# Optimization experiments

Hardware: AMD Instinct MI355X
Metric: run time of the kernel (lower is better)

The kernel has to match this reference:

```python
import jax, jax.numpy as jnp
import numpy as np

B, C_IN, T = 64, 9, 4096
HIDDEN, OUT = 128, 10
NEW_T = T // 4            # two MaxPool1d(2) stages
N_NODES = B * NEW_T       # 65536 flattened nodes
N_EDGES = 524288


def setup_inputs() -> dict:
    key = jax.random.key(0)
    ks = jax.random.split(key, 8)
    def w(k, sh, fan):
        return jax.random.normal(k, sh, jnp.float32) * (1.0 / np.sqrt(fan))
    return {
        "x": jax.random.normal(ks[0], (B, C_IN, T), jnp.float32),
        "edge_index": jax.random.randint(ks[1], (2, N_EDGES), 0, N_NODES, dtype=jnp.int32),
        "conv1_w": w(ks[2], (16, C_IN, 5), C_IN * 5),
        "conv1_b": jnp.zeros((16,), jnp.float32),
        "conv2_w": w(ks[3], (32, 16, 5), 16 * 5),
        "conv2_b": jnp.zeros((32,), jnp.float32),
        "gcn1_w": w(ks[4], (32, HIDDEN), 32),
        "gcn1_b": jnp.zeros((HIDDEN,), jnp.float32),
        "gcn2_w": w(ks[5], (HIDDEN, HIDDEN), HIDDEN),
        "gcn2_b": jnp.zeros((HIDDEN,), jnp.float32),
        "cls_w": w(ks[6], (HIDDEN, OUT), HIDDEN),
        "cls_b": jnp.zeros((OUT,), jnp.float32),
    }


def _conv1d(x, w, b):
    # x: [B, C, T], w: [O, I, K], 'same' padding (pad=2, k=5)
    y = jax.lax.conv_general_dilated(x, w, (1,), [(2, 2)],
                                     dimension_numbers=("NCH", "OIH", "NCH"))
    return y + b[None, :, None]


def _maxpool2(x):
    return jax.lax.reduce_window(x, -jnp.inf, jax.lax.max, (1, 1, 2), (1, 1, 2), "VALID")


def _gcn(x, w, b, src, dst):
    # PyG GCNConv: add self-loops, symmetric D^{-1/2}(A+I)D^{-1/2} X W + b
    h = x @ w
    deg = jnp.zeros((N_NODES,), x.dtype).at[dst].add(1.0) + 1.0  # +1 for self-loop
    dinv = jax.lax.rsqrt(deg)
    coef = dinv[src] * dinv[dst]                      # [E]
    agg = jnp.zeros_like(h).at[dst].add(h[src] * coef[:, None])
    agg = agg + h * (dinv * dinv)[:, None]            # self-loop contribution
    return agg + b


def reference(x, edge_index, conv1_w, conv1_b, conv2_w, conv2_b,
              gcn1_w, gcn1_b, gcn2_w, gcn2_b, cls_w, cls_b):
    h = _maxpool2(jax.nn.relu(_conv1d(x, conv1_w, conv1_b)))   # [B,16,T/2]
    h = _maxpool2(jax.nn.relu(_conv1d(h, conv2_w, conv2_b)))   # [B,32,T/4]
    feats = h.transpose(0, 2, 1).reshape(-1, 32)               # [B*NEW_T, 32]
    src, dst = edge_index[0], edge_index[1]
    g = jax.nn.relu(_gcn(feats, gcn1_w, gcn1_b, src, dst))
    g = jax.nn.relu(_gcn(g, gcn2_w, gcn2_b, src, dst))
    pooled = g.reshape(B, NEW_T, HIDDEN).mean(axis=1)          # mean over nodes per graph
    return pooled @ cls_w + cls_b                              # [B, OUT]
```

## Files before the change

kernel.cpp:

```cpp
#include <hip/hip_runtime.h>
#include <hip/hip_bf16.h>

typedef __hip_bfloat16 bf16;
typedef unsigned short ushort8_v __attribute__((ext_vector_type(8)));
typedef short bf16x8 __attribute__((ext_vector_type(8)));
typedef float f32x4 __attribute__((ext_vector_type(4)));
typedef float f32x2 __attribute__((ext_vector_type(2)));

#define N_B     64
#define C_IN    9
#define T0      4096
#define C1      16
#define T1      2048
#define C2      32
#define T2      1024
#define N_NODES 65536
#define N_EDGES 524288
#define HID     128
#define OUT_C   10
#define SLOT_CAP 32

__device__ __forceinline__ float us2f(unsigned short u) {
  union { unsigned int i; float f; } c; c.i = ((unsigned int)u) << 16; return c.f;
}
__device__ __forceinline__ unsigned short f2us(float f) {
  bf16 h = __float2bfloat16(f);
  unsigned short u;
  __builtin_memcpy(&u, &h, 2);
  return u;
}
__device__ __forceinline__ unsigned char f2fp8(float f) {
  int p = __builtin_amdgcn_cvt_pk_fp8_f32(f, f, 0, false);
  return (unsigned char)(p & 0xFF);
}
__device__ __forceinline__ void fp8w_to_f32x4(unsigned int w, float* out) {
  f32x2 lo = __builtin_amdgcn_cvt_pk_f32_fp8((int)w, false);
  f32x2 hi = __builtin_amdgcn_cvt_pk_f32_fp8((int)w, true);
  out[0] = lo[0]; out[1] = lo[1]; out[2] = hi[0]; out[3] = hi[1];
}

__global__ __launch_bounds__(256) void conv1_scatter_kernel(const float* __restrict__ x, const float* __restrict__ w1,
                                                            const float* __restrict__ b1,
                                                            const int* __restrict__ ei, int* __restrict__ cnt,
                                                            unsigned short* __restrict__ slots,
                                                            unsigned short* __restrict__ y1,
                                                            const float* __restrict__ W1, const float* __restrict__ W2,
                                                            unsigned short* __restrict__ W1T,
                                                            unsigned short* __restrict__ W2T,
                                                            float* __restrict__ pooled)
{
  __shared__ float sx[C_IN * 136];
  __shared__ float sw[45 * 17];
  __shared__ float sb[C1];
  int tid = threadIdx.x;
  if (blockIdx.x < 2048) {
    int e = blockIdx.x * 256 + tid;
    int d = ei[N_EDGES + e];
    int s = ei[e];
    int r = atomicAdd(&cnt[d], 1);
    if (r < SLOT_CAP) slots[((size_t)d << 5) + r] = (unsigned short)s;
    return;
  }
  if (blockIdx.x >= 4096) {
    int blk = blockIdx.x - 4096;
    if (blk < 16) {
      int base = blk * 1024 + tid * 4;
      #pragma unroll
      for (int i = 0; i < 4; ++i) {
        int idx = base + i;
        int j = idx >> 7, k = idx & 127;
        W2T[j * HID + k] = f2us(W2[(size_t)k * HID + j]);
      }
    } else {
      #pragma unroll
      for (int i = 0; i < 16; ++i) {
        int idx = tid * 16 + i;
        int j = idx >> 5, k = idx & 31;
        W1T[j * 32 + k] = f2us(W1[(size_t)k * HID + j]);
      }
      float4 z4 = make_float4(0.f, 0.f, 0.f, 0.f);
      for (int i = tid; i < N_B * HID / 4; i += 256)
        ((float4*)pooled)[i] = z4;
    }
    return;
  }
  int blk = blockIdx.x - 2048;
  int b = blk >> 5;
  int P0 = (blk & 31) << 6;
  int t0 = 2 * P0 - 2;
  for (int i = tid; i < C_IN * 132; i += 256) {
    int c = i / 132, j = i % 132;
    int t = t0 + j;
    sx[c * 136 + j] = (t >= 0 && t < T0) ? x[(size_t)(b * C_IN + c) * T0 + t] : 0.f;
  }
  for (int i = tid; i < C1 * 45; i += 256) sw[(i % 45) * 17 + i / 45] = w1[i];
  if (tid < C1) sb[tid] = b1[tid];
  __syncthreads();

  int o = tid & 15, pg = tid >> 4;
  float bias = sb[o];
  float a[8];
  #pragma unroll
  for (int i = 0; i < 8; ++i) a[i] = bias;
  #pragma unroll
  for (int c = 0; c < C_IN; ++c) {
    float xv[12];
    #pragma unroll
    for (int q = 0; q < 3; ++q)
      *(float4*)&xv[4 * q] = *(const float4*)&sx[c * 136 + 8 * pg + 4 * q];
    const float* wr = &sw[(c * 5) * 17 + o];
    float w0 = wr[0], w1_ = wr[17], w2_ = wr[34], w3_ = wr[51], w4_ = wr[68];
    #pragma unroll
    for (int m = 0; m < 8; ++m)
      a[m] += xv[m]*w0 + xv[m+1]*w1_ + xv[m+2]*w2_ + xv[m+3]*w3_ + xv[m+4]*w4_;
  }
  ushort4 r;
  r.x = f2us(fmaxf(fmaxf(a[0], a[1]), 0.f));
  r.y = f2us(fmaxf(fmaxf(a[2], a[3]), 0.f));
  r.z = f2us(fmaxf(fmaxf(a[4], a[5]), 0.f));
  r.w = f2us(fmaxf(fmaxf(a[6], a[7]), 0.f));
  *(ushort4*)&y1[(size_t)(b * C1 + o) * T1 + P0 + 4 * pg] = r;
}

__global__ __launch_bounds__(256) void conv2_kernel(const unsigned short* __restrict__ y1, const float* __restrict__ w2,
                                                    const float* __restrict__ b2, const int* __restrict__ cnt,
                                                    unsigned short* __restrict__ feats)
{
  __shared__ float sy[C1 * 72];
  __shared__ float sw[80 * 33];
  __shared__ float sb[C2];
  int tid = threadIdx.x;
  int b = blockIdx.x >> 5;
  int Q0 = (blockIdx.x & 31) << 5;
  int t0 = 2 * Q0 - 2;
  for (int i = tid; i < C1 * 68; i += 256) {
    int c = i / 68, j = i % 68;
    int t = t0 + j;
    sy[c * 72 + j] = (t >= 0 && t < T1) ? us2f(y1[(size_t)(b * C1 + c) * T1 + t]) : 0.f;
  }
  for (int i = tid; i < C2 * 80; i += 256) sw[(i % 80) * 33 + i / 80] = w2[i];
  if (tid < C2) sb[tid] = b2[tid];
  __syncthreads();

  int o = tid & 31, pg = tid >> 5;
  float bias = sb[o];
  float a[8];
  #pragma unroll
  for (int i = 0; i < 8; ++i) a[i] = bias;
  #pragma unroll
  for (int c = 0; c < C1; ++c) {
    float yv[12];
    #pragma unroll
    for (int q = 0; q < 3; ++q)
      *(float4*)&yv[4 * q] = *(const float4*)&sy[c * 72 + 8 * pg + 4 * q];
    const float* wr = &sw[(c * 5) * 33 + o];
    float w0 = wr[0], w1_ = wr[33], w2_ = wr[66], w3_ = wr[99], w4_ = wr[132];
    #pragma unroll
    for (int m = 0; m < 8; ++m)
      a[m] += yv[m]*w0 + yv[m+1]*w1_ + yv[m+2]*w2_ + yv[m+3]*w3_ + yv[m+4]*w4_;
  }
  #pragma unroll
  for (int i = 0; i < 4; ++i) {
    int node = (b << 10) + Q0 + 4 * pg + i;
    float dv = rsqrtf((float)cnt[node] + 1.0f);
    feats[(size_t)node * C2 + o] = f2us(fmaxf(fmaxf(a[2*i], a[2*i+1]), 0.f) * dv);
  }
}

__global__ __launch_bounds__(256) void gemm12_kernel(const unsigned short* __restrict__ F,
                                                     const int* __restrict__ cnt,
                                                     const unsigned short* __restrict__ slots,
                                                     const unsigned short* __restrict__ W1T,
                                                     const float* __restrict__ gb1,
                                                     const unsigned short* __restrict__ W2T,
                                                     unsigned char* __restrict__ Hb)
{
  __shared__ unsigned short sG[64 * 132];
  int tid = threadIdx.x;
  int w = tid >> 6, l = tid & 63;
  int lr = l & 15, lk = l >> 4;
  int n0b = blockIdx.x << 6;
  int jb = w << 5;

  {
    int nb = w << 4;
    int node = n0b + nb + lr;
    int cn = cnt[node];
    float dn = rsqrtf((float)cn + 1.0f);
    int koff = lk << 3;
    float accf[8];
    {
      ushort8_v r = *(const ushort8_v*)(F + (size_t)node * C2 + koff);
      #pragma unroll
      for (int k = 0; k < 8; ++k) accf[k] = us2f(r[k]);
    }
    const unsigned short* sl = slots + ((size_t)node << 5);
    int e1 = min(cn, SLOT_CAP);
    int e = 0;
    for (; e + 4 <= e1; e += 4) {
      int s0 = sl[e], s1 = sl[e + 1], s2 = sl[e + 2], s3 = sl[e + 3];
      ushort8_v r0 = *(const ushort8_v*)(F + (size_t)s0 * C2 + koff);
      ushort8_v r1 = *(const ushort8_v*)(F + (size_t)s1 * C2 + koff);
      ushort8_v r2 = *(const ushort8_v*)(F + (size_t)s2 * C2 + koff);
      ushort8_v r3 = *(const ushort8_v*)(F + (size_t)s3 * C2 + koff);
      #pragma unroll
      for (int k = 0; k < 8; ++k)
        accf[k] += (us2f(r0[k]) + us2f(r1[k])) + (us2f(r2[k]) + us2f(r3[k]));
    }
    for (; e < e1; ++e) {
      int s0 = sl[e];
      ushort8_v r0 = *(const ushort8_v*)(F + (size_t)s0 * C2 + koff);
      #pragma unroll
      for (int k = 0; k < 8; ++k) accf[k] += us2f(r0[k]);
    }
    bf16x8 af;
    #pragma unroll
    for (int k = 0; k < 8; ++k) af[k] = (short)f2us(accf[k] * dn);

    #pragma unroll
    for (int jt = 0; jt < 8; ++jt) {
      bf16x8 bfr = *(const bf16x8*)((const short*)W1T + (jt * 16 + lr) * 32 + lk * 8);
      f32x4 acc = {0.f, 0.f, 0.f, 0.f};
      acc = __builtin_amdgcn_mfma_f32_16x16x32_bf16(af, bfr, acc, 0, 0, 0);
      float bj = gb1[jt * 16 + lr];
      #pragma unroll
      for (int r = 0; r < 4; ++r)
        sG[(nb + lk * 4 + r) * 132 + jt * 16 + lr] = f2us(fmaxf(acc[r] + bj, 0.f));
    }
  }

  bf16x8 bfr[2][4];
  #pragma unroll
  for (int jtt = 0; jtt < 2; ++jtt)
    #pragma unroll
    for (int ks = 0; ks < 4; ++ks)
      bfr[jtt][ks] = *(const bf16x8*)((const short*)W2T + (size_t)(jb + jtt * 16 + lr) * HID + ks * 32 + lk * 8);

  __syncthreads();

  {
    #pragma unroll
    for (int nt = 0; nt < 4; ++nt) {
      bf16x8 afr[4];
      #pragma unroll
      for (int ks = 0; ks < 4; ++ks)
        afr[ks] = *(const bf16x8*)((const short*)sG + (nt * 16 + lr) * 132 + ks * 32 + lk * 8);
      int rowb = n0b + nt * 16 + lk * 4;
      int4 c4 = *(const int4*)&cnt[rowb];
      float dvr[4] = { rsqrtf((float)c4.x + 1.f), rsqrtf((float)c4.y + 1.f),
                       rsqrtf((float)c4.z + 1.f), rsqrtf((float)c4.w + 1.f) };
      #pragma unroll
      for (int jtt = 0; jtt < 2; ++jtt) {
        f32x4 acc = {0.f, 0.f, 0.f, 0.f};
        #pragma unroll
        for (int ks = 0; ks < 4; ++ks)
          acc = __builtin_amdgcn_mfma_f32_16x16x32_bf16(afr[ks], bfr[jtt][ks], acc, 0, 0, 0);
        #pragma unroll
        for (int r = 0; r < 4; ++r)
          Hb[(size_t)(rowb + r) * HID + jb + jtt * 16 + lr] = f2fp8(acc[r] * dvr[r]);
      }
    }
  }
}

__global__ __launch_bounds__(256) void agg2_pool_kernel(const unsigned char* __restrict__ Hb, const int* __restrict__ cnt,
                                                        const unsigned short* __restrict__ slots,
                                                        const float* __restrict__ bias, float* __restrict__ pooled)
{
  __shared__ float red[16][HID];
  int tid = threadIdx.x;
  int g = tid >> 4;
  int jq = (tid & 15) << 3;
  int node = (blockIdx.x << 4) + g;
  int cn = cnt[node];
  float dn = rsqrtf((float)cn + 1.0f);
  float acc[8];
  {
    uint2 v = *(const uint2*)(Hb + (size_t)node * HID + jq);
    fp8w_to_f32x4(v.x, &acc[0]);
    fp8w_to_f32x4(v.y, &acc[4]);
  }
  const unsigned short* sl = slots + ((size_t)node << 5);
  int e1 = min(cn, SLOT_CAP);
  int e = 0;
  for (; e + 4 <= e1; e += 4) {
    uint2 v0 = *(const uint2*)(Hb + (size_t)sl[e]     * HID + jq);
    uint2 v1 = *(const uint2*)(Hb + (size_t)sl[e + 1] * HID + jq);
    uint2 v2 = *(const uint2*)(Hb + (size_t)sl[e + 2] * HID + jq);
    uint2 v3 = *(const uint2*)(Hb + (size_t)sl[e + 3] * HID + jq);
    float t0[8], t1[8], t2[8], t3[8];
    fp8w_to_f32x4(v0.x, &t0[0]); fp8w_to_f32x4(v0.y, &t0[4]);
    fp8w_to_f32x4(v1.x, &t1[0]); fp8w_to_f32x4(v1.y, &t1[4]);
    fp8w_to_f32x4(v2.x, &t2[0]); fp8w_to_f32x4(v2.y, &t2[4]);
    fp8w_to_f32x4(v3.x, &t3[0]); fp8w_to_f32x4(v3.y, &t3[4]);
    #pragma unroll
    for (int k = 0; k < 8; ++k)
      acc[k] += (t0[k] + t1[k]) + (t2[k] + t3[k]);
  }
  for (; e < e1; ++e) {
    uint2 v0 = *(const uint2*)(Hb + (size_t)sl[e] * HID + jq);
    float t0[8];
    fp8w_to_f32x4(v0.x, &t0[0]); fp8w_to_f32x4(v0.y, &t0[4]);
    #pragma unroll
    for (int k = 0; k < 8; ++k) acc[k] += t0[k];
  }
  #pragma unroll
  for (int k = 0; k < 8; ++k)
    red[g][jq + k] = fmaxf(dn * acc[k] + bias[jq + k], 0.f);
  __syncthreads();
  if (tid < HID) {
    float s = 0.f;
    #pragma unroll
    for (int g2 = 0; g2 < 16; ++g2) s += red[g2][tid];
    int b = blockIdx.x >> 6;
    atomicAdd(&pooled[b * HID + tid], s * (1.0f / 1024.0f));
  }
}


__global__ __launch_bounds__(64) void cls_kernel(const float* __restrict__ pooled, const float* __restrict__ w,
                                                 const float* __restrict__ cb, float* __restrict__ out)
{
  int b = blockIdx.x, o = threadIdx.x;
  if (o < OUT_C) {
    float acc = cb[o];
    for (int i = 0; i < HID; ++i)
      acc += pooled[b * HID + i] * w[i * OUT_C + o];
    out[b * OUT_C + o] = acc;
  }
}


extern "C" void kernel_launch(void* const* d_in, const int* in_sizes, int n_in,
                              void* d_out, int out_size, void* d_ws, size_t ws_size,
                              hipStream_t stream)
{
  const float* x    = (const float*)d_in[0];
  const int*   ei   = (const int*)d_in[1];
  const float* c1w  = (const float*)d_in[2];
  const float* c1b  = (const float*)d_in[3];
  const float* c2w  = (const float*)d_in[4];
  const float* c2b  = (const float*)d_in[5];
  const float* g1w  = (const float*)d_in[6];
  const float* g1b  = (const float*)d_in[7];
  const float* g2w  = (const float*)d_in[8];
  const float* g2b  = (const float*)d_in[9];
  const float* clsw = (const float*)d_in[10];
  const float* clsb = (const float*)d_in[11];
  float* outp = (float*)d_out;

  char* ws = (char*)d_ws;
  size_t off_b = 0;
  auto alloc = [&](size_t bytes) { void* p = ws + off_b; off_b = (off_b + bytes + 255) & ~(size_t)255; return p; };
  int*   cnt    = (int*)  alloc((size_t)N_NODES * 4);
  unsigned short* slots = (unsigned short*)alloc((size_t)N_NODES * SLOT_CAP * 2);
  unsigned short* w1t   = (unsigned short*)alloc((size_t)HID * 32 * 2);
  unsigned short* w2t   = (unsigned short*)alloc((size_t)HID * HID * 2);
  unsigned short* y1    = (unsigned short*)alloc((size_t)N_B * C1 * T1 * 2);
  unsigned short* feats = (unsigned short*)alloc((size_t)N_NODES * C2 * 2);
  unsigned char*  H     = (unsigned char*) alloc((size_t)N_NODES * HID);
  float* pooled = (float*)alloc((size_t)N_B * HID * 4);
  (void)ws_size; (void)in_sizes; (void)n_in; (void)out_size;

  hipMemsetAsync(cnt, 0, (size_t)N_NODES * 4, stream);

  conv1_scatter_kernel<<<4113, 256, 0, stream>>>(x, c1w, c1b, ei, cnt, slots, y1, g1w, g2w, w1t, w2t, pooled);

  conv2_kernel<<<2048, 256, 0, stream>>>(y1, c2w, c2b, cnt, feats);

  gemm12_kernel<<<N_NODES / 64, 256, 0, stream>>>(feats, cnt, slots, w1t, g1b, w2t, H);

  agg2_pool_kernel<<<N_NODES / 16, 256, 0, stream>>>(H, cnt, slots, g2b, pooled);

  cls_kernel<<<N_B, 64, 0, stream>>>(pooled, clsw, clsb, outp);
}
```

Baseline: 98.35 us.

## Fuse conv1 and conv2 into one front kernel, move source-degree scaling to gather

```diff
diff --git a/kernel.cpp b/kernel.cpp
--- a/kernel.cpp
+++ b/kernel.cpp
@@ -39,20 +39,25 @@
   out[0] = lo[0]; out[1] = lo[1]; out[2] = hi[0]; out[3] = hi[1];
 }
 
-__global__ __launch_bounds__(256) void conv1_scatter_kernel(const float* __restrict__ x, const float* __restrict__ w1,
-                                                            const float* __restrict__ b1,
-                                                            const int* __restrict__ ei, int* __restrict__ cnt,
-                                                            unsigned short* __restrict__ slots,
-                                                            unsigned short* __restrict__ y1,
-                                                            const float* __restrict__ W1, const float* __restrict__ W2,
-                                                            unsigned short* __restrict__ W1T,
-                                                            unsigned short* __restrict__ W2T,
-                                                            float* __restrict__ pooled)
-{
-  __shared__ float sx[C_IN * 136];
-  __shared__ float sw[45 * 17];
-  __shared__ float sb[C1];
+__global__ __launch_bounds__(256) void front_kernel(const float* __restrict__ x, const float* __restrict__ w1c,
+                                                    const float* __restrict__ b1c, const float* __restrict__ w2c,
+                                                    const float* __restrict__ b2c,
+                                                    const int* __restrict__ ei, int* __restrict__ cnt,
+                                                    unsigned short* __restrict__ slots,
+                                                    const float* __restrict__ W1, const float* __restrict__ W2,
+                                                    unsigned short* __restrict__ W1T,
+                                                    unsigned short* __restrict__ W2T,
+                                                    float* __restrict__ pooled,
+                                                    unsigned short* __restrict__ feats)
+{
+  __shared__ float sx[C_IN * 144];
+  __shared__ float sy[C1 * 72];
+  __shared__ float sw1[45 * 17];
+  __shared__ float sw2[80 * 33];
+  __shared__ float sb1[C1];
+  __shared__ float sb2[C2];
   int tid = threadIdx.x;
+
   if (blockIdx.x < 2048) {
     int e = blockIdx.x * 256 + tid;
     int d = ei[N_EDGES + e];
@@ -84,86 +89,92 @@
     }
     return;
   }
+
   int blk = blockIdx.x - 2048;
   int b = blk >> 5;
-  int P0 = (blk & 31) << 6;
-  int t0 = 2 * P0 - 2;
-  for (int i = tid; i < C_IN * 132; i += 256) {
-    int c = i / 132, j = i % 132;
-    int t = t0 + j;
-    sx[c * 136 + j] = (t >= 0 && t < T0) ? x[(size_t)(b * C_IN + c) * T0 + t] : 0.f;
-  }
-  for (int i = tid; i < C1 * 45; i += 256) sw[(i % 45) * 17 + i / 45] = w1[i];
-  if (tid < C1) sb[tid] = b1[tid];
+  int Q0 = (blk & 31) << 5;
+  int x0 = 4 * Q0 - 6;
+
+  for (int i = tid; i < C_IN * 140; i += 256) {
+    int c = i / 140, j = i % 140;
+    int t = x0 + j;
+    sx[c * 144 + j] = (t >= 0 && t < T0) ? x[(size_t)(b * C_IN + c) * T0 + t] : 0.f;
+  }
+  for (int i = tid; i < C1 * 45; i += 256) sw1[(i % 45) * 17 + i / 45] = w1c[i];
+  for (int i = tid; i < C2 * 80; i += 256) sw2[(i % 80) * 33 + i / 80] = w2c[i];
+  if (tid < C1) sb1[tid] = b1c[tid];
+  else if (tid >= 32 && tid < 64) sb2[tid - 32] = b2c[tid - 32];
   __syncthreads();
 
-  int o = tid & 15, pg = tid >> 4;
-  float bias = sb[o];
-  float a[8];
-  #pragma unroll
-  for (int i = 0; i < 8; ++i) a[i] = bias;
-  #pragma unroll
-  for (int c = 0; c < C_IN; ++c) {
-    float xv[12];
-    #pragma unroll
-    for (int q = 0; q < 3; ++q)
-      *(float4*)&xv[4 * q] = *(const float4*)&sx[c * 136 + 8 * pg + 4 * q];
-    const float* wr = &sw[(c * 5) * 17 + o];
-    float w0 = wr[0], w1_ = wr[17], w2_ = wr[34], w3_ = wr[51], w4_ = wr[68];
-    #pragma unroll
-    for (int m = 0; m < 8; ++m)
-      a[m] += xv[m]*w0 + xv[m+1]*w1_ + xv[m+2]*w2_ + xv[m+3]*w3_ + xv[m+4]*w4_;
-  }
-  ushort4 r;
-  r.x = f2us(fmaxf(fmaxf(a[0], a[1]), 0.f));
-  r.y = f2us(fmaxf(fmaxf(a[2], a[3]), 0.f));
-  r.z = f2us(fmaxf(fmaxf(a[4], a[5]), 0.f));
-  r.w = f2us(fmaxf(fmaxf(a[6], a[7]), 0.f));
-  *(ushort4*)&y1[(size_t)(b * C1 + o) * T1 + P0 + 4 * pg] = r;
-}
-
-__global__ __launch_bounds__(256) void conv2_kernel(const unsigned short* __restrict__ y1, const float* __restrict__ w2,
-                                                    const float* __restrict__ b2, const int* __restrict__ cnt,
-                                                    unsigned short* __restrict__ feats)
-{
-  __shared__ float sy[C1 * 72];
-  __shared__ float sw[80 * 33];
-  __shared__ float sb[C2];
-  int tid = threadIdx.x;
-  int b = blockIdx.x >> 5;
-  int Q0 = (blockIdx.x & 31) << 5;
-  int t0 = 2 * Q0 - 2;
-  for (int i = tid; i < C1 * 68; i += 256) {
-    int c = i / 68, j = i % 68;
-    int t = t0 + j;
-    sy[c * 72 + j] = (t >= 0 && t < T1) ? us2f(y1[(size_t)(b * C1 + c) * T1 + t]) : 0.f;
-  }
-  for (int i = tid; i < C2 * 80; i += 256) sw[(i % 80) * 33 + i / 80] = w2[i];
-  if (tid < C2) sb[tid] = b2[tid];
+  {
+    int o = tid & 15, pg = tid >> 4;
+    float bias = sb1[o];
+    float a[8];
+    #pragma unroll
+    for (int i = 0; i < 8; ++i) a[i] = bias;
+    #pragma unroll
+    for (int c = 0; c < C_IN; ++c) {
+      float xv[12];
+      #pragma unroll
+      for (int q = 0; q < 3; ++q)
+        *(float4*)&xv[4 * q] = *(const float4*)&sx[c * 144 + 8 * pg + 4 * q];
+      const float* wr = &sw1[(c * 5) * 17 + o];
+      float w0 = wr[0], w1_ = wr[17], w2_ = wr[34], w3_ = wr[51], w4_ = wr[68];
+      #pragma unroll
+      for (int m = 0; m < 8; ++m)
+        a[m] += xv[m]*w0 + xv[m+1]*w1_ + xv[m+2]*w2_ + xv[m+3]*w3_ + xv[m+4]*w4_;
+    }
+    float4 r;
+    int pb = 2 * Q0 - 2 + 4 * pg;
+    r.x = (pb + 0 >= 0 && pb + 0 < T1) ? fmaxf(fmaxf(a[0], a[1]), 0.f) : 0.f;
+    r.y = (pb + 1 >= 0 && pb + 1 < T1) ? fmaxf(fmaxf(a[2], a[3]), 0.f) : 0.f;
+    r.z = (pb + 2 >= 0 && pb + 2 < T1) ? fmaxf(fmaxf(a[4], a[5]), 0.f) : 0.f;
+    r.w = (pb + 3 >= 0 && pb + 3 < T1) ? fmaxf(fmaxf(a[6], a[7]), 0.f) : 0.f;
+    *(float4*)&sy[o * 72 + 4 * pg] = r;
+    if (pg < 4) {
+      int q = 64 + pg;
+      int p = 2 * Q0 - 2 + q;
+      float v = 0.f;
+      if (p >= 0 && p < T1) {
+        float t0 = bias, t1 = bias;
+        #pragma unroll
+        for (int c = 0; c < C_IN; ++c) {
+          const float* xr = &sx[c * 144 + 2 * q];
+          const float* wr = &sw1[(c * 5) * 17 + o];
+          float w0 = wr[0], w1_ = wr[17], w2_ = wr[34], w3_ = wr[51], w4_ = wr[68];
+          t0 += xr[0]*w0 + xr[1]*w1_ + xr[2]*w2_ + xr[3]*w3_ + xr[4]*w4_;
+          t1 += xr[1]*w0 + xr[2]*w1_ + xr[3]*w2_ + xr[4]*w3_ + xr[5]*w4_;
+        }
+        v = fmaxf(fmaxf(t0, t1), 0.f);
+      }
+      sy[o * 72 + q] = v;
+    }
+  }
   __syncthreads();
 
-  int o = tid & 31, pg = tid >> 5;
-  float bias = sb[o];
-  float a[8];
-  #pragma unroll
-  for (int i = 0; i < 8; ++i) a[i] = bias;
-  #pragma unroll
-  for (int c = 0; c < C1; ++c) {
-    float yv[12];
-    #pragma unroll
-    for (int q = 0; q < 3; ++q)
-      *(float4*)&yv[4 * q] = *(const float4*)&sy[c * 72 + 8 * pg + 4 * q];
-    const float* wr = &sw[(c * 5) * 33 + o];
-    float w0 = wr[0], w1_ = wr[33], w2_ = wr[66], w3_ = wr[99], w4_ = wr[132];
-    #pragma unroll
-    for (int m = 0; m < 8; ++m)
-      a[m] += yv[m]*w0 + yv[m+1]*w1_ + yv[m+2]*w2_ + yv[m+3]*w3_ + yv[m+4]*w4_;
-  }
-  #pragma unroll
-  for (int i = 0; i < 4; ++i) {
-    int node = (b << 10) + Q0 + 4 * pg + i;
-    float dv = rsqrtf((float)cnt[node] + 1.0f);
-    feats[(size_t)node * C2 + o] = f2us(fmaxf(fmaxf(a[2*i], a[2*i+1]), 0.f) * dv);
+  {
+    int o = tid & 31, ug = tid >> 5;
+    float bias = sb2[o];
+    float a[8];
+    #pragma unroll
+    for (int i = 0; i < 8; ++i) a[i] = bias;
+    #pragma unroll
+    for (int c = 0; c < C1; ++c) {
+      float yv[12];
+      #pragma unroll
+      for (int q = 0; q < 3; ++q)
+        *(float4*)&yv[4 * q] = *(const float4*)&sy[c * 72 + 8 * ug + 4 * q];
+      const float* wr = &sw2[(c * 5) * 33 + o];
+      float w0 = wr[0], w1_ = wr[33], w2_ = wr[66], w3_ = wr[99], w4_ = wr[132];
+      #pragma unroll
+      for (int m = 0; m < 8; ++m)
+        a[m] += yv[m]*w0 + yv[m+1]*w1_ + yv[m+2]*w2_ + yv[m+3]*w3_ + yv[m+4]*w4_;
+    }
+    #pragma unroll
+    for (int i = 0; i < 4; ++i) {
+      int node = (b << 10) + Q0 + 4 * ug + i;
+      feats[(size_t)node * C2 + o] = f2us(fmaxf(fmaxf(a[2*i], a[2*i+1]), 0.f));
+    }
   }
 }
 
@@ -192,26 +203,29 @@
     {
       ushort8_v r = *(const ushort8_v*)(F + (size_t)node * C2 + koff);
       #pragma unroll
-      for (int k = 0; k < 8; ++k) accf[k] = us2f(r[k]);
+      for (int k = 0; k < 8; ++k) accf[k] = us2f(r[k]) * dn;
     }
     const unsigned short* sl = slots + ((size_t)node << 5);
     int e1 = min(cn, SLOT_CAP);
     int e = 0;
     for (; e + 4 <= e1; e += 4) {
       int s0 = sl[e], s1 = sl[e + 1], s2 = sl[e + 2], s3 = sl[e + 3];
+      float d0 = rsqrtf((float)cnt[s0] + 1.f), d1 = rsqrtf((float)cnt[s1] + 1.f);
+      float d2 = rsqrtf((float)cnt[s2] + 1.f), d3 = rsqrtf((float)cnt[s3] + 1.f);
       ushort8_v r0 = *(const ushort8_v*)(F + (size_t)s0 * C2 + koff);
       ushort8_v r1 = *(const ushort8_v*)(F + (size_t)s1 * C2 + koff);
       ushort8_v r2 = *(const ushort8_v*)(F + (size_t)s2 * C2 + koff);
       ushort8_v r3 = *(const ushort8_v*)(F + (size_t)s3 * C2 + koff);
       #pragma unroll
       for (int k = 0; k < 8; ++k)
-        accf[k] += (us2f(r0[k]) + us2f(r1[k])) + (us2f(r2[k]) + us2f(r3[k]));
+        accf[k] += (us2f(r0[k]) * d0 + us2f(r1[k]) * d1) + (us2f(r2[k]) * d2 + us2f(r3[k]) * d3);
     }
     for (; e < e1; ++e) {
       int s0 = sl[e];
+      float d0 = rsqrtf((float)cnt[s0] + 1.f);
       ushort8_v r0 = *(const ushort8_v*)(F + (size_t)s0 * C2 + koff);
       #pragma unroll
-      for (int k = 0; k < 8; ++k) accf[k] += us2f(r0[k]);
+      for (int k = 0; k < 8; ++k) accf[k] += us2f(r0[k]) * d0;
     }
     bf16x8 af;
     #pragma unroll
@@ -356,7 +370,6 @@
   unsigned short* slots = (unsigned short*)alloc((size_t)N_NODES * SLOT_CAP * 2);
   unsigned short* w1t   = (unsigned short*)alloc((size_t)HID * 32 * 2);
   unsigned short* w2t   = (unsigned short*)alloc((size_t)HID * HID * 2);
-  unsigned short* y1    = (unsigned short*)alloc((size_t)N_B * C1 * T1 * 2);
   unsigned short* feats = (unsigned short*)alloc((size_t)N_NODES * C2 * 2);
   unsigned char*  H     = (unsigned char*) alloc((size_t)N_NODES * HID);
   float* pooled = (float*)alloc((size_t)N_B * HID * 4);
@@ -364,9 +377,8 @@
 
   hipMemsetAsync(cnt, 0, (size_t)N_NODES * 4, stream);
 
-  conv1_scatter_kernel<<<4113, 256, 0, stream>>>(x, c1w, c1b, ei, cnt, slots, y1, g1w, g2w, w1t, w2t, pooled);
-
-  conv2_kernel<<<2048, 256, 0, stream>>>(y1, c2w, c2b, cnt, feats);
+  front_kernel<<<4113, 256, 0, stream>>>(x, c1w, c1b, c2w, c2b, ei, cnt, slots,
+                                         g1w, g2w, w1t, w2t, pooled, feats);
 
   gemm12_kernel<<<N_NODES / 64, 256, 0, stream>>>(feats, cnt, slots, w1t, g1b, w2t, H);
 
```

Result: faster. 96.24 us (-2.1%).
